# Kernel optimization log

Measured on AMD Instinct MI355X. Metric: run time of the kernel, lower is better.

## Reference

```python
import jax, jax.numpy as jnp
import numpy as np

S = 4096      # packed sequence length
DIM = 1024    # model dim
H = 8         # num heads
HD = 64       # per-branch head dim (head_dim // 2 in the module)
LAMBDA_INIT = 0.8 - 0.6 * float(np.exp(-0.3 * 0.0))  # depth=0 -> 0.2
EPS = 1e-5


def setup_inputs() -> dict:
    key = jax.random.key(0)
    ks = jax.random.split(key, 10)
    P = 2 * H * HD  # = 1024
    return {
        "x": jax.random.normal(ks[0], (S, DIM), jnp.float32),
        "mask": jnp.ones((1, 1, S, S), jnp.bool_),
        "Wq": jax.random.normal(ks[1], (DIM, P), jnp.float32) * 0.02,
        "Wk": jax.random.normal(ks[2], (DIM, P), jnp.float32) * 0.02,
        "Wv": jax.random.normal(ks[3], (DIM, P), jnp.float32) * 0.02,
        "Wo": jax.random.normal(ks[4], (P, DIM), jnp.float32) * 0.02,
        "lambda_q1": jax.random.normal(ks[5], (HD,), jnp.float32) * 0.1,
        "lambda_k1": jax.random.normal(ks[6], (HD,), jnp.float32) * 0.1,
        "lambda_q2": jax.random.normal(ks[7], (HD,), jnp.float32) * 0.1,
        "lambda_k2": jax.random.normal(ks[8], (HD,), jnp.float32) * 0.1,
        "subln_weight": jnp.ones((2 * HD,), jnp.float32),
    }


def reference(x, mask, Wq, Wk, Wv, Wo, lambda_q1, lambda_k1, lambda_q2,
              lambda_k2, subln_weight):
    # projections: (S, 2H, HD) split into branch index along a new axis
    xq = (x @ Wq).reshape(S, H, 2, HD)   # [2*H] view -> (H,2) contiguous split
    xk = (x @ Wk).reshape(S, H, 2, HD)
    xv = (x @ Wv).reshape(S, H, 2 * HD)
    q1, q2 = xq[:, :, 0], xq[:, :, 1]    # (S,H,HD)
    k1, k2 = xk[:, :, 0], xk[:, :, 1]

    scale = 1.0 / jnp.sqrt(jnp.float32(HD))
    bias = jnp.where(mask[0, 0], 0.0, -jnp.inf)  # (S,S) additive mask

    def sdpa(q, k):
        # q,k: (S,H,HD); xv: (S,H,2HD)
        scores = jnp.einsum('shd,thd->hst', q, k) * scale + bias  # (H,S,S)
        p = jax.nn.softmax(scores, axis=-1)
        return jnp.einsum('hst,thd->shd', p, xv)                  # (S,H,2HD)

    attn1 = sdpa(q1, k1)
    attn2 = sdpa(q2, k2)

    lam1 = jnp.exp(jnp.sum(lambda_q1 * lambda_k1))
    lam2 = jnp.exp(jnp.sum(lambda_q2 * lambda_k2))
    lambda_full = lam1 - lam2 + LAMBDA_INIT

    attn = attn1 - lambda_full * attn2                            # (S,H,2HD)
    # RMSNorm over last dim (2*HD) with learnable weight
    attn = attn * jax.lax.rsqrt(jnp.mean(attn * attn, axis=-1, keepdims=True) + EPS)
    attn = attn * subln_weight
    attn = attn * (1.0 - LAMBDA_INIT)
    return attn.reshape(S, H * 2 * HD) @ Wo                       # (S, DIM)
```

## Files before the change

kernel.cpp:

```cpp
#include <hip/hip_runtime.h>
#include <hip/hip_bf16.h>
#include <type_traits>
#include <utility>


using bf16 = __hip_bfloat16;

static constexpr int SQ = 4096;
static constexpr int DM = 1024;
static constexpr float LAMB_INIT = 0.2f;
static constexpr float KSC = 0.18033688011112043f;

typedef float  f32x4    __attribute__((ext_vector_type(4)));
typedef short  s16x4    __attribute__((ext_vector_type(4)));
typedef short  bf16x8_i __attribute__((ext_vector_type(8)));
typedef __bf16 bf16x8_b __attribute__((ext_vector_type(8)));

template<typename T, typename = void> struct mfma_ok : std::false_type {};
template<typename T> struct mfma_ok<T, std::void_t<decltype(
    __builtin_amdgcn_mfma_f32_16x16x32_bf16(std::declval<T>(), std::declval<T>(),
                                            std::declval<f32x4>(), 0, 0, 0))>>
    : std::true_type {};
using abfrag = std::conditional_t<mfma_ok<bf16x8_b>::value, bf16x8_b, bf16x8_i>;

__device__ __forceinline__ f32x4 mfma16(abfrag a, abfrag b, f32x4 c) {
    return __builtin_amdgcn_mfma_f32_16x16x32_bf16(a, b, c, 0, 0, 0);
}
__device__ __forceinline__ abfrag ldfrag(const bf16* p) {
    return *reinterpret_cast<const abfrag*>(p);
}
__device__ __forceinline__ short bf2s(bf16 b) {
    short s; __builtin_memcpy(&s, &b, 2); return s;
}
__device__ __forceinline__ float fexp2(float x) {
#if __has_builtin(__builtin_amdgcn_exp2f)
    return __builtin_amdgcn_exp2f(x);
#else
    return exp2f(x);
#endif
}
__device__ __forceinline__ void gld_lds16(const bf16* g, bf16* l) {
    __builtin_amdgcn_global_load_lds((__attribute__((address_space(1))) void*)g,
                                     (__attribute__((address_space(3))) void*)l,
                                     16, 0, 0);
}


__global__ __launch_bounds__(256) void convert_x(const float* __restrict__ in,
                                                 bf16* __restrict__ outp)
{
    const size_t i = ((size_t)blockIdx.x * 256 + threadIdx.x) * 4;
    const f32x4 v = *reinterpret_cast<const f32x4*>(in + i);
    s16x4 o;
#pragma unroll
    for (int j = 0; j < 4; ++j) o[j] = bf2s(__float2bfloat16(v[j]));
    *reinterpret_cast<s16x4*>(outp + i) = o;
}

__global__ __launch_bounds__(256) void transpose_w(
    const float* __restrict__ Wq, const float* __restrict__ Wk,
    const float* __restrict__ Wv, const float* __restrict__ Wo,
    bf16* __restrict__ Wqt, bf16* __restrict__ Wkt,
    bf16* __restrict__ Wvt, bf16* __restrict__ Wot)
{
    const int z = blockIdx.z;
    const float* src = (z == 0) ? Wq : (z == 1) ? Wk : (z == 2) ? Wv : Wo;
    bf16* dst        = (z == 0) ? Wqt : (z == 1) ? Wkt : (z == 2) ? Wvt : Wot;
    const float scale = (z == 0) ? KSC : 1.0f;
    __shared__ float tbuf[32][33];
    const int k0 = blockIdx.x * 32, n0 = blockIdx.y * 32;
    const int c = threadIdx.x & 31, r0 = threadIdx.x >> 5;
#pragma unroll
    for (int i = 0; i < 4; ++i)
        tbuf[r0 + i * 8][c] = src[(size_t)(k0 + r0 + i * 8) * 1024 + n0 + c];
    __syncthreads();
#pragma unroll
    for (int i = 0; i < 4; ++i)
        dst[(size_t)(n0 + r0 + i * 8) * 1024 + k0 + c] =
            __float2bfloat16(tbuf[c][r0 + i * 8] * scale);
}

__global__ __launch_bounds__(256) void transpose_v(const bf16* __restrict__ V,
                                                   bf16* __restrict__ Vt)
{
    __shared__ bf16 tbuf[32][33];
    const int s0 = blockIdx.x * 32, n0 = blockIdx.y * 32;
    const int c = threadIdx.x & 31, r0 = threadIdx.x >> 5;
#pragma unroll
    for (int i = 0; i < 4; ++i)
        tbuf[r0 + i * 8][c] = V[(size_t)(s0 + r0 + i * 8) * 1024 + n0 + c];
    __syncthreads();
#pragma unroll
    for (int i = 0; i < 4; ++i)
        Vt[(size_t)(n0 + r0 + i * 8) * 4096 + s0 + c] = tbuf[c][r0 + i * 8];
}

__global__ void lambda_kernel(const float* lq1, const float* lk1,
                              const float* lq2, const float* lk2, float* outp)
{
    const int lane = threadIdx.x;
    float a = lq1[lane] * lk1[lane];
    float b = lq2[lane] * lk2[lane];
#pragma unroll
    for (int m = 1; m < 64; m <<= 1) {
        a += __shfl_xor(a, m, 64);
        b += __shfl_xor(b, m, 64);
    }
    if (lane == 0) outp[0] = __expf(a) - __expf(b) + LAMB_INIT;
}


template<bool BF16OUT>
__device__ __forceinline__ void gemm_core(const bf16* __restrict__ A,
                                          const bf16* __restrict__ Bt,
                                          void* __restrict__ Cout,
                                          int m0, int n0, int ldc)
{
    __shared__ __align__(16) bf16 As[128 * 32];
    __shared__ __align__(16) bf16 Bs[128 * 32];
    const int tid  = threadIdx.x;
    const int wid  = tid >> 6;
    const int lane = tid & 63;
    const int l15  = lane & 15;
    const int l4   = lane >> 4;
    const int wr   = wid >> 1;
    const int wc   = wid & 1;

    const f32x4 zero4 = {0.f, 0.f, 0.f, 0.f};
    f32x4 acc[4][4];
#pragma unroll
    for (int i = 0; i < 4; ++i)
#pragma unroll
        for (int j = 0; j < 4; ++j) acc[i][j] = zero4;

    for (int kt = 0; kt < 1024; kt += 32) {
        __syncthreads();
#pragma unroll
        for (int it = 0; it < 2; ++it) {
            const int flat = it * 256 + tid;
            const int row  = flat >> 2;
            const int c16  = flat & 3;
            const int ldst = (it * 256 + wid * 64) * 8;
            gld_lds16(&A [(size_t)(m0 + row) * 1024 + kt + c16 * 8], &As[ldst]);
            gld_lds16(&Bt[(size_t)(n0 + row) * 1024 + kt + c16 * 8], &Bs[ldst]);
        }
        __syncthreads();
        abfrag a[4], b[4];
#pragma unroll
        for (int mi = 0; mi < 4; ++mi)
            a[mi] = ldfrag(&As[(wr * 64 + mi * 16 + l15) * 32 + l4 * 8]);
#pragma unroll
        for (int ni = 0; ni < 4; ++ni)
            b[ni] = ldfrag(&Bs[(wc * 64 + ni * 16 + l15) * 32 + l4 * 8]);
#pragma unroll
        for (int mi = 0; mi < 4; ++mi)
#pragma unroll
            for (int ni = 0; ni < 4; ++ni)
                acc[mi][ni] = mfma16(a[mi], b[ni], acc[mi][ni]);
    }

#pragma unroll
    for (int mi = 0; mi < 4; ++mi)
#pragma unroll
        for (int ni = 0; ni < 4; ++ni)
#pragma unroll
            for (int r = 0; r < 4; ++r) {
                const int row = m0 + wr * 64 + mi * 16 + l4 * 4 + r;
                const int col = n0 + wc * 64 + ni * 16 + l15;
                if constexpr (BF16OUT)
                    ((bf16*)Cout)[(size_t)row * ldc + col] = __float2bfloat16(acc[mi][ni][r]);
                else
                    ((float*)Cout)[(size_t)row * ldc + col] = acc[mi][ni][r];
            }
}

__global__ __launch_bounds__(256, 2) void gemm_qkv(
    const bf16* __restrict__ xbf,
    const bf16* __restrict__ Wqt, const bf16* __restrict__ Wkt,
    const bf16* __restrict__ Wvt,
    bf16* __restrict__ Qo, bf16* __restrict__ Ko, bf16* __restrict__ Vo)
{
    const int which = blockIdx.y >> 3;
    const bf16* Bt = (which == 0) ? Wqt : (which == 1) ? Wkt : Wvt;
    bf16* Cp       = (which == 0) ? Qo  : (which == 1) ? Ko  : Vo;
    gemm_core<true>(xbf, Bt, Cp, blockIdx.x * 128, (blockIdx.y & 7) * 128, 1024);
}

__global__ __launch_bounds__(256, 2) void gemm_out(
    const bf16* __restrict__ Amat, const bf16* __restrict__ Wot,
    float* __restrict__ out)
{
    gemm_core<false>(Amat, Wot, out, blockIdx.x * 128, blockIdx.y * 128, 1024);
}


__global__ __launch_bounds__(256, 2) void flash_diff(
    const bf16* __restrict__ Qm, const bf16* __restrict__ Km,
    const bf16* __restrict__ Vtm, const float* __restrict__ lam_ptr,
    const float* __restrict__ subln, bf16* __restrict__ Amat)
{
    const int bid  = blockIdx.x;
    const int h    = bid & 7;
    const int qt   = bid >> 3;
    const int tid  = threadIdx.x;
    const int wid  = tid >> 6;
    const int lane = tid & 63;
    const int l15  = lane & 15;
    const int l4   = lane >> 4;
    const int qbase = qt * 64 + wid * 16;
    const int swz   = (l15 & 7) << 4;

    constexpr float THR = 8.0f;

    __shared__ __align__(16) bf16 KB[2][64 * 128];
    __shared__ __align__(16) bf16 VB[2][128 * 64];

    abfrag qf[2][2];
#pragma unroll
    for (int c = 0; c < 2; ++c)
#pragma unroll
        for (int kc = 0; kc < 2; ++kc)
            qf[c][kc] = ldfrag(&Qm[(size_t)(qbase + l15) * DM +
                                   h * 128 + c * 64 + kc * 32 + l4 * 8]);

    union { abfrag f; short s[8]; } uon;
#pragma unroll
    for (int i = 0; i < 8; ++i) uon.s[i] = (short)0x3F80;
    const abfrag ones = uon.f;

    const bf16* kap[4];
    const bf16* vap[4];
#pragma unroll
    for (int it = 0; it < 4; ++it) {
        const int slot = it * 256 + tid;
        const int krow = slot >> 4;
        const int kscb = ((slot & 15) << 4) ^ ((krow & 7) << 4);
        kap[it] = &Km[(size_t)krow * DM + h * 128 + (kscb >> 1)];
        const int vrow = slot >> 3;
        const int vscb = ((slot & 7) << 4) ^ ((vrow & 7) << 4);
        vap[it] = &Vtm[(size_t)(h * 128 + vrow) * SQ + (vscb >> 1)];
    }
    auto stage = [&](int buf) {
#pragma unroll
        for (int it = 0; it < 4; ++it) {
            gld_lds16(kap[it], &KB[buf][(it * 256 + wid * 64) * 8]);
            gld_lds16(vap[it], &VB[buf][(it * 256 + wid * 64) * 8]);
            kap[it] += 64 * DM;
            vap[it] += 64;
        }
    };

    const f32x4 zero4 = {0.f, 0.f, 0.f, 0.f};
    f32x4 o_[2][8];
#pragma unroll
    for (int c = 0; c < 2; ++c)
#pragma unroll
        for (int vt = 0; vt < 8; ++vt) o_[c][vt] = zero4;
    f32x4 lacc[2] = {zero4, zero4};
    float m_loc[2] = {0.f, 0.f};

    stage(0);
    __syncthreads();

    int cur = 0;
    constexpr int NT = SQ / 64;
#pragma unroll 1
    for (int t = 0; t < NT; ++t) {
        if (t + 1 < NT) stage(cur ^ 1);

        const char* kb = (const char*)KB[cur];
        const char* vb = (const char*)VB[cur];

        abfrag pa[2][2];
#pragma unroll
        for (int c = 0; c < 2; ++c) {
            const float mc = m_loc[c];
            const f32x4 binit = {-mc, -mc, -mc, -mc};
            f32x4 sc[4];
#pragma unroll
            for (int j = 0; j < 4; ++j) {
                const char* kr = kb + (j * 16 + l15) * 256;
                const abfrag k0 = *(const abfrag*)(kr + ((c * 128 + l4 * 16) ^ swz));
                const abfrag k1 = *(const abfrag*)(kr + ((c * 128 + 64 + l4 * 16) ^ swz));
                f32x4 z = mfma16(k0, qf[c][0], binit);
                sc[j] = mfma16(k1, qf[c][1], z);
            }
            float lmx = fmaxf(fmaxf(sc[0][0], sc[0][1]), fmaxf(sc[0][2], sc[0][3]));
#pragma unroll
            for (int j = 1; j < 4; ++j)
                lmx = fmaxf(lmx, fmaxf(fmaxf(sc[j][0], sc[j][1]),
                                       fmaxf(sc[j][2], sc[j][3])));
            if (__any(lmx > THR)) {
                float mx = lmx;
                mx = fmaxf(mx, __shfl_xor(mx, 16, 64));
                mx = fmaxf(mx, __shfl_xor(mx, 32, 64));
                const float alpha = fexp2(-mx);
                m_loc[c] += mx;
#pragma unroll
                for (int r = 0; r < 4; ++r) {
                    const float alr = __shfl(alpha, l4 * 4 + r, 64);
#pragma unroll
                    for (int vt = 0; vt < 8; ++vt) o_[c][vt][r] *= alr;
                    lacc[c][r] *= alr;
                }
#pragma unroll
                for (int j = 0; j < 4; ++j)
#pragma unroll
                    for (int r = 0; r < 4; ++r) sc[j][r] -= mx;
            }
            f32x4 pe[4];
#pragma unroll
            for (int j = 0; j < 4; ++j)
#pragma unroll
                for (int r = 0; r < 4; ++r) pe[j][r] = fexp2(sc[j][r]);
            union { abfrag f; short s[8]; } u0, u1;
#pragma unroll
            for (int r = 0; r < 4; ++r) {
                u0.s[r]     = bf2s(__float2bfloat16(pe[0][r]));
                u0.s[4 + r] = bf2s(__float2bfloat16(pe[1][r]));
                u1.s[r]     = bf2s(__float2bfloat16(pe[2][r]));
                u1.s[4 + r] = bf2s(__float2bfloat16(pe[3][r]));
            }
            pa[c][0] = u0.f;
            pa[c][1] = u1.f;
        }

        __builtin_amdgcn_s_setprio(1);
        lacc[0] = mfma16(pa[0][0], ones, lacc[0]);
        lacc[0] = mfma16(pa[0][1], ones, lacc[0]);
        lacc[1] = mfma16(pa[1][0], ones, lacc[1]);
        lacc[1] = mfma16(pa[1][1], ones, lacc[1]);
#pragma unroll
        for (int vt = 0; vt < 8; ++vt) {
            const char* vr = vb + (vt * 16 + l15) * 128;
#pragma unroll
            for (int ch = 0; ch < 2; ++ch) {
                union { abfrag f; s16x4 hh[2]; } vv;
                vv.hh[0] = *(const s16x4*)(vr + ((ch * 64 + l4 * 8) ^ swz));
                vv.hh[1] = *(const s16x4*)(vr + ((ch * 64 + 32 + l4 * 8) ^ swz));
                o_[0][vt] = mfma16(pa[0][ch], vv.f, o_[0][vt]);
                o_[1][vt] = mfma16(pa[1][ch], vv.f, o_[1][vt]);
            }
        }
        __builtin_amdgcn_s_setprio(0);

        __syncthreads();
        cur ^= 1;
    }

    const float lam = lam_ptr[0];
    float il1[4], il2[4];
#pragma unroll
    for (int r = 0; r < 4; ++r) {
        il1[r] = 1.f / lacc[0][r];
        il2[r] = lam / lacc[1][r];
    }
#pragma unroll
    for (int r = 0; r < 4; ++r) {
        float comb[8];
        float ss = 0.f;
#pragma unroll
        for (int vt = 0; vt < 8; ++vt) {
            const float v = o_[0][vt][r] * il1[r] - o_[1][vt][r] * il2[r];
            comb[vt] = v;
            ss += v * v;
        }
        ss += __shfl_xor(ss, 1, 64);
        ss += __shfl_xor(ss, 2, 64);
        ss += __shfl_xor(ss, 4, 64);
        ss += __shfl_xor(ss, 8, 64);
        const float rinv = rsqrtf(ss * (1.f / 128.f) + 1e-5f);
        const int row = qbase + l4 * 4 + r;
#pragma unroll
        for (int vt = 0; vt < 8; ++vt) {
            const float outv = comb[vt] * rinv * subln[vt * 16 + l15] * 0.8f;
            Amat[(size_t)row * DM + h * 128 + vt * 16 + l15] = __float2bfloat16(outv);
        }
    }
}


extern "C" void kernel_launch(void* const* d_in, const int* in_sizes, int n_in,
                              void* d_out, int out_size, void* d_ws, size_t ws_size,
                              hipStream_t stream)
{
    (void)in_sizes; (void)n_in; (void)out_size; (void)ws_size;
    const float* x    = (const float*)d_in[0];
    const float* Wq   = (const float*)d_in[2];
    const float* Wk   = (const float*)d_in[3];
    const float* Wv   = (const float*)d_in[4];
    const float* Wo   = (const float*)d_in[5];
    const float* lq1  = (const float*)d_in[6];
    const float* lk1  = (const float*)d_in[7];
    const float* lq2  = (const float*)d_in[8];
    const float* lk2  = (const float*)d_in[9];
    const float* subw = (const float*)d_in[10];

    char* ws = (char*)d_ws;
    size_t off = 0;
    auto take = [&](size_t n) { void* p = ws + off; off += (n + 255) & ~(size_t)255; return p; };
    bf16* xbf = (bf16*)take((size_t)SQ * DM * 2);
    bf16* Wqt = (bf16*)take((size_t)DM * DM * 2);
    bf16* Wkt = (bf16*)take((size_t)DM * DM * 2);
    bf16* Wvt = (bf16*)take((size_t)DM * DM * 2);
    bf16* Wot = (bf16*)take((size_t)DM * DM * 2);
    bf16* Qb  = (bf16*)take((size_t)SQ * DM * 2);
    bf16* Kb  = (bf16*)take((size_t)SQ * DM * 2);
    bf16* Vb  = (bf16*)take((size_t)SQ * DM * 2);
    bf16* Vtb = (bf16*)take((size_t)SQ * DM * 2);
    bf16* Am  = (bf16*)take((size_t)SQ * DM * 2);
    float* lamp = (float*)take(256);

    convert_x   <<<dim3(SQ * DM / 1024), dim3(256), 0, stream>>>(x, xbf);
    transpose_w <<<dim3(32, 32, 4),      dim3(256), 0, stream>>>(Wq, Wk, Wv, Wo, Wqt, Wkt, Wvt, Wot);
    lambda_kernel<<<dim3(1),             dim3(64),  0, stream>>>(lq1, lk1, lq2, lk2, lamp);
    gemm_qkv    <<<dim3(32, 24),         dim3(256), 0, stream>>>(xbf, Wqt, Wkt, Wvt, Qb, Kb, Vb);
    transpose_v <<<dim3(128, 32),        dim3(256), 0, stream>>>(Vb, Vtb);
    flash_diff  <<<dim3(512),            dim3(256), 0, stream>>>(Qb, Kb, Vtb, lamp, subw, Am);
    gemm_out    <<<dim3(32, 8),          dim3(256), 0, stream>>>(Am, Wot, (float*)d_out);
}
```

Baseline: 194.9 us.

## Triple-buffer K/V staging with 512-thread blocks and packed bf16 conversion

The flash attention kernel now uses 8 waves per block covering 128 query rows, so each staged K/V tile is shared by twice as many queries. Staging moves from double to triple buffering, with explicit vmcnt waits and raw barriers so loads run two tiles ahead. LDS lane offsets are precomputed, and probability-to-bf16 conversion uses the packed v_cvt_pk_bf16_f32 instruction. The grid halves to 256 blocks, which may underfill the CUs, and the 96KB LDS per block limits how many blocks fit on each CU.

```diff
diff --git a/kernel.cpp b/kernel.cpp
--- a/kernel.cpp
+++ b/kernel.cpp
@@ -38,6 +38,11 @@
 #else
     return exp2f(x);
 #endif
+}
+__device__ __forceinline__ int cvtpk(float lo, float hi) {
+    int r;
+    asm("v_cvt_pk_bf16_f32 %0, %1, %2" : "=v"(r) : "v"(lo), "v"(hi));
+    return r;
 }
 __device__ __forceinline__ void gld_lds16(const bf16* g, bf16* l) {
     __builtin_amdgcn_global_load_lds((__attribute__((address_space(1))) void*)g,
@@ -194,7 +199,7 @@
 }
 
 
-__global__ __launch_bounds__(256, 2) void flash_diff(
+__global__ __launch_bounds__(512, 2) void flash_diff(
     const bf16* __restrict__ Qm, const bf16* __restrict__ Km,
     const bf16* __restrict__ Vtm, const float* __restrict__ lam_ptr,
     const float* __restrict__ subln, bf16* __restrict__ Amat)
@@ -207,13 +212,13 @@
     const int lane = tid & 63;
     const int l15  = lane & 15;
     const int l4   = lane >> 4;
-    const int qbase = qt * 64 + wid * 16;
+    const int qbase = qt * 128 + wid * 16;
     const int swz   = (l15 & 7) << 4;
 
     constexpr float THR = 8.0f;
-
-    __shared__ __align__(16) bf16 KB[2][64 * 128];
-    __shared__ __align__(16) bf16 VB[2][128 * 64];
+    constexpr int KOFF = 0, VOFF = 49152, BUFSZ = 16384;
+
+    __shared__ __align__(16) char smem[98304];
 
     abfrag qf[2][2];
 #pragma unroll
@@ -222,33 +227,45 @@
         for (int kc = 0; kc < 2; ++kc)
             qf[c][kc] = ldfrag(&Qm[(size_t)(qbase + l15) * DM +
                                    h * 128 + c * 64 + kc * 32 + l4 * 8]);
+    asm volatile("" :: "v"(qf[0][0]), "v"(qf[0][1]), "v"(qf[1][0]), "v"(qf[1][1]));
 
     union { abfrag f; short s[8]; } uon;
 #pragma unroll
     for (int i = 0; i < 8; ++i) uon.s[i] = (short)0x3F80;
     const abfrag ones = uon.f;
 
-    const bf16* kap[4];
-    const bf16* vap[4];
-#pragma unroll
-    for (int it = 0; it < 4; ++it) {
-        const int slot = it * 256 + tid;
+    const bf16* kap[2];
+    const bf16* vap[2];
+#pragma unroll
+    for (int it = 0; it < 2; ++it) {
+        const int slot = it * 512 + tid;
         const int krow = slot >> 4;
-        const int kscb = ((slot & 15) << 4) ^ ((krow & 7) << 4);
-        kap[it] = &Km[(size_t)krow * DM + h * 128 + (kscb >> 1)];
+        const int kcb  = ((slot & 15) << 4) ^ ((krow & 7) << 4);
+        kap[it] = Km + (size_t)krow * DM + h * 128 + (kcb >> 1);
         const int vrow = slot >> 3;
-        const int vscb = ((slot & 7) << 4) ^ ((vrow & 7) << 4);
-        vap[it] = &Vtm[(size_t)(h * 128 + vrow) * SQ + (vscb >> 1)];
+        const int vcb  = ((slot & 7) << 4) ^ ((vrow & 7) << 4);
+        vap[it] = Vtm + (size_t)(h * 128 + vrow) * SQ + (vcb >> 1);
     }
     auto stage = [&](int buf) {
-#pragma unroll
-        for (int it = 0; it < 4; ++it) {
-            gld_lds16(kap[it], &KB[buf][(it * 256 + wid * 64) * 8]);
-            gld_lds16(vap[it], &VB[buf][(it * 256 + wid * 64) * 8]);
+        char* kd = smem + KOFF + buf * BUFSZ;
+        char* vd = smem + VOFF + buf * BUFSZ;
+#pragma unroll
+        for (int it = 0; it < 2; ++it) {
+            gld_lds16(kap[it], (bf16*)(kd + (it * 512 + wid * 64) * 16));
             kap[it] += 64 * DM;
+            gld_lds16(vap[it], (bf16*)(vd + (it * 512 + wid * 64) * 16));
             vap[it] += 64;
         }
     };
+
+    const int kLane0 = l15 * 256 + ((l4 * 16) ^ swz);
+    const int kLane1 = l15 * 256 + ((64 + l4 * 16) ^ swz);
+    int vLane[4];
+#pragma unroll
+    for (int ch = 0; ch < 2; ++ch)
+#pragma unroll
+        for (int hh = 0; hh < 2; ++hh)
+            vLane[ch * 2 + hh] = l15 * 128 + ((ch * 64 + hh * 32 + l4 * 8) ^ swz);
 
     const f32x4 zero4 = {0.f, 0.f, 0.f, 0.f};
     f32x4 o_[2][8];
@@ -260,16 +277,21 @@
     float m_loc[2] = {0.f, 0.f};
 
     stage(0);
-    __syncthreads();
-
-    int cur = 0;
+    stage(1);
+    asm volatile("s_waitcnt vmcnt(4)" ::: "memory");
+    __builtin_amdgcn_s_barrier();
+
+    int cur = 0, nxt = 2;
     constexpr int NT = SQ / 64;
 #pragma unroll 1
     for (int t = 0; t < NT; ++t) {
-        if (t + 1 < NT) stage(cur ^ 1);
-
-        const char* kb = (const char*)KB[cur];
-        const char* vb = (const char*)VB[cur];
+        const bool pf = (t + 2 < NT);
+        if (pf) stage(nxt);
+
+        const char* kbuf = smem + KOFF + cur * BUFSZ;
+        const char* vbuf = smem + VOFF + cur * BUFSZ;
+        const char* kb0  = kbuf + kLane0;
+        const char* kb1  = kbuf + kLane1;
 
         abfrag pa[2][2];
 #pragma unroll
@@ -279,9 +301,8 @@
             f32x4 sc[4];
 #pragma unroll
             for (int j = 0; j < 4; ++j) {
-                const char* kr = kb + (j * 16 + l15) * 256;
-                const abfrag k0 = *(const abfrag*)(kr + ((c * 128 + l4 * 16) ^ swz));
-                const abfrag k1 = *(const abfrag*)(kr + ((c * 128 + 64 + l4 * 16) ^ swz));
+                const abfrag k0 = *(const abfrag*)(kb0 + (j * 4096 + c * 128));
+                const abfrag k1 = *(const abfrag*)(kb1 + (j * 4096 + c * 128));
                 f32x4 z = mfma16(k0, qf[c][0], binit);
                 sc[j] = mfma16(k1, qf[c][1], z);
             }
@@ -313,17 +334,23 @@
             for (int j = 0; j < 4; ++j)
 #pragma unroll
                 for (int r = 0; r < 4; ++r) pe[j][r] = fexp2(sc[j][r]);
-            union { abfrag f; short s[8]; } u0, u1;
-#pragma unroll
-            for (int r = 0; r < 4; ++r) {
-                u0.s[r]     = bf2s(__float2bfloat16(pe[0][r]));
-                u0.s[4 + r] = bf2s(__float2bfloat16(pe[1][r]));
-                u1.s[r]     = bf2s(__float2bfloat16(pe[2][r]));
-                u1.s[4 + r] = bf2s(__float2bfloat16(pe[3][r]));
-            }
+            union { abfrag f; int i[4]; } u0, u1;
+            u0.i[0] = cvtpk(pe[0][0], pe[0][1]);
+            u0.i[1] = cvtpk(pe[0][2], pe[0][3]);
+            u0.i[2] = cvtpk(pe[1][0], pe[1][1]);
+            u0.i[3] = cvtpk(pe[1][2], pe[1][3]);
+            u1.i[0] = cvtpk(pe[2][0], pe[2][1]);
+            u1.i[1] = cvtpk(pe[2][2], pe[2][3]);
+            u1.i[2] = cvtpk(pe[3][0], pe[3][1]);
+            u1.i[3] = cvtpk(pe[3][2], pe[3][3]);
             pa[c][0] = u0.f;
             pa[c][1] = u1.f;
         }
+
+        const char* vb00 = vbuf + vLane[0];
+        const char* vb01 = vbuf + vLane[1];
+        const char* vb10 = vbuf + vLane[2];
+        const char* vb11 = vbuf + vLane[3];
 
         __builtin_amdgcn_s_setprio(1);
         lacc[0] = mfma16(pa[0][0], ones, lacc[0]);
@@ -332,20 +359,23 @@
         lacc[1] = mfma16(pa[1][1], ones, lacc[1]);
 #pragma unroll
         for (int vt = 0; vt < 8; ++vt) {
-            const char* vr = vb + (vt * 16 + l15) * 128;
-#pragma unroll
-            for (int ch = 0; ch < 2; ++ch) {
-                union { abfrag f; s16x4 hh[2]; } vv;
-                vv.hh[0] = *(const s16x4*)(vr + ((ch * 64 + l4 * 8) ^ swz));
-                vv.hh[1] = *(const s16x4*)(vr + ((ch * 64 + 32 + l4 * 8) ^ swz));
-                o_[0][vt] = mfma16(pa[0][ch], vv.f, o_[0][vt]);
-                o_[1][vt] = mfma16(pa[1][ch], vv.f, o_[1][vt]);
-            }
+            union { abfrag f; s16x4 hh[2]; } v0, v1;
+            v0.hh[0] = *(const s16x4*)(vb00 + vt * 2048);
+            v0.hh[1] = *(const s16x4*)(vb01 + vt * 2048);
+            v1.hh[0] = *(const s16x4*)(vb10 + vt * 2048);
+            v1.hh[1] = *(const s16x4*)(vb11 + vt * 2048);
+            o_[0][vt] = mfma16(pa[0][0], v0.f, o_[0][vt]);
+            o_[1][vt] = mfma16(pa[1][0], v0.f, o_[1][vt]);
+            o_[0][vt] = mfma16(pa[0][1], v1.f, o_[0][vt]);
+            o_[1][vt] = mfma16(pa[1][1], v1.f, o_[1][vt]);
         }
         __builtin_amdgcn_s_setprio(0);
 
-        __syncthreads();
-        cur ^= 1;
+        if (pf) asm volatile("s_waitcnt vmcnt(4)" ::: "memory");
+        else    asm volatile("s_waitcnt vmcnt(0)" ::: "memory");
+        __builtin_amdgcn_s_barrier();
+        cur = (cur == 2) ? 0 : cur + 1;
+        nxt = (nxt == 2) ? 0 : nxt + 1;
     }
 
     const float lam = lam_ptr[0];
@@ -416,6 +446,6 @@
     lambda_kernel<<<dim3(1),             dim3(64),  0, stream>>>(lq1, lk1, lq2, lk2, lamp);
     gemm_qkv    <<<dim3(32, 24),         dim3(256), 0, stream>>>(xbf, Wqt, Wkt, Wvt, Qb, Kb, Vb);
     transpose_v <<<dim3(128, 32),        dim3(256), 0, stream>>>(Vb, Vtb);
-    flash_diff  <<<dim3(512),            dim3(256), 0, stream>>>(Qb, Kb, Vtb, lamp, subw, Am);
+    flash_diff  <<<dim3(256),            dim3(512), 0, stream>>>(Qb, Kb, Vtb, lamp, subw, Am);
     gemm_out    <<<dim3(32, 8),          dim3(256), 0, stream>>>(Am, Wot, (float*)d_out);
 }
```

Result: no change. 192.8 us (-1.0%).
